# Performance work log

Measured on AMD Instinct MI355X. Metric: run time of the kernel, lower is better.

## Reference

```python
import jax, jax.numpy as jnp
import numpy as np

B, D, E, K, H, C = 8192, 1024, 8, 2, 2048, 512
LN_EPS = 1e-5


def setup_inputs() -> dict:
    key = jax.random.key(0)
    ks = jax.random.split(key, 6)
    s = 0.02
    return {
        "x": jax.random.normal(ks[0], (B, D), dtype=jnp.float32),
        "Wr": jax.random.normal(ks[1], (E, D), dtype=jnp.float32) * s,  # router weight [E,D]
        "br": jnp.zeros((E,), dtype=jnp.float32),
        "gamma": jnp.ones((E, D), dtype=jnp.float32),   # per-expert LayerNorm scale
        "beta": jnp.zeros((E, D), dtype=jnp.float32),   # per-expert LayerNorm shift
        "W1": jax.random.normal(ks[2], (E, H, D), dtype=jnp.float32) * s,
        "b1": jnp.zeros((E, H), dtype=jnp.float32),
        "W2": jax.random.normal(ks[3], (E, C, H), dtype=jnp.float32) * s,
        "b2": jnp.zeros((E, C), dtype=jnp.float32),
    }


def reference(x, Wr, br, gamma, beta, W1, b1, W2, b2):
    # Router + top-k gating (softmax over the k selected logits only)
    router_logits = x @ Wr.T + br                       # [B,E]
    topk_vals, topk_idx = jax.lax.top_k(router_logits, K)  # [B,K]
    topk_w = jax.nn.softmax(topk_vals, axis=-1)         # [B,K]
    # Dense gate [B,E]: gate[b,e] = sum_j topk_w[b,j] * (topk_idx[b,j]==e)
    gate = (jax.nn.one_hot(topk_idx, E, dtype=x.dtype) * topk_w[..., None]).sum(axis=1)

    # LayerNorm statistics are expert-independent; affine is per-expert
    mu = x.mean(axis=-1, keepdims=True)
    var = ((x - mu) ** 2).mean(axis=-1, keepdims=True)
    xn = (x - mu) * jax.lax.rsqrt(var + LN_EPS)          # [B,D]

    out = jnp.zeros((x.shape[0], C), dtype=x.dtype)
    for e in range(E):  # small fixed expert count
        xe = xn * gamma[e] + beta[e]                     # [B,D]
        h = jax.nn.gelu(xe @ W1[e].T + b1[e], approximate=False)  # [B,H]
        y = h @ W2[e].T + b2[e]                          # [B,C]
        out = out + gate[:, e:e + 1] * y
    return out
```

## Files before the change

### kernel.cpp

```cpp
#include <hip/hip_runtime.h>
#include <hip/hip_bf16.h>
#include <math.h>

#define B_TOK 8192
#define DDIM 1024
#define NEXP 8
#define HDIM 2048
#define CDIM 512
#define LN_EPS 1e-5f
#define MAXT256 72
#define MAXROWS (MAXT256 * 256)

typedef __attribute__((ext_vector_type(4))) float f32x4;
typedef __attribute__((ext_vector_type(8))) short bf16x8;

__device__ __forceinline__ unsigned short f2bf(float f) {
  __hip_bfloat16 h = __float2bfloat16(f);
  return *reinterpret_cast<unsigned short*>(&h);
}
__device__ __forceinline__ float bf2f(unsigned short u) {
  unsigned int x = ((unsigned int)u) << 16;
  return *reinterpret_cast<float*>(&x);
}

__device__ __forceinline__ float gelu_f(float v) {
  const float t = __builtin_fmaf(0.044715f * v, v, 1.0f);
  const float u = -1.5957691216f * v * t;
  return v * __builtin_amdgcn_rcpf(1.0f + __expf(u));
}

__device__ __forceinline__ void gload_lds16(const unsigned short* g, unsigned short* l) {
  __builtin_amdgcn_global_load_lds(
      (const __attribute__((address_space(1))) unsigned int*)g,
      (__attribute__((address_space(3))) unsigned int*)l, 16, 0, 0);
}

__global__ __launch_bounds__(256) void router_ln_kernel(
    const float* __restrict__ x, const float* __restrict__ Wr,
    const float* __restrict__ br, int* __restrict__ eidx,
    float* __restrict__ wgt, unsigned short* __restrict__ xn) {
  const int wid = threadIdx.x >> 6;
  const int lane = threadIdx.x & 63;
  const int tok = blockIdx.x * 4 + wid;

  const float4* xr = reinterpret_cast<const float4*>(x + (size_t)tok * DDIM);
  float4 xv[4];
  float sum = 0.f, sumsq = 0.f;
  float dot[NEXP];
#pragma unroll
  for (int e = 0; e < NEXP; ++e) dot[e] = 0.f;

#pragma unroll
  for (int i = 0; i < 4; ++i) {
    const int f = i * 64 + lane;
    float4 v = xr[f];
    xv[i] = v;
    sum += v.x + v.y + v.z + v.w;
    sumsq += v.x * v.x + v.y * v.y + v.z * v.z + v.w * v.w;
#pragma unroll
    for (int e = 0; e < NEXP; ++e) {
      float4 w = reinterpret_cast<const float4*>(Wr + e * DDIM)[f];
      dot[e] += v.x * w.x + v.y * w.y + v.z * w.z + v.w * w.w;
    }
  }
#pragma unroll
  for (int off = 32; off > 0; off >>= 1) {
    sum += __shfl_xor(sum, off);
    sumsq += __shfl_xor(sumsq, off);
#pragma unroll
    for (int e = 0; e < NEXP; ++e) dot[e] += __shfl_xor(dot[e], off);
  }
  const float mu = sum * (1.f / DDIM);
  const float var = sumsq * (1.f / DDIM) - mu * mu;
  const float rs = rsqrtf(var + LN_EPS);

  float lg[NEXP];
#pragma unroll
  for (int e = 0; e < NEXP; ++e) lg[e] = dot[e] + br[e];

  int i1 = 0; float v1 = lg[0];
#pragma unroll
  for (int e = 1; e < NEXP; ++e) { if (lg[e] > v1) { v1 = lg[e]; i1 = e; } }
  int i2 = -1; float v2 = -3.4e38f;
#pragma unroll
  for (int e = 0; e < NEXP; ++e) { if (e != i1 && lg[e] > v2) { v2 = lg[e]; i2 = e; } }

  const float e2 = __expf(v2 - v1);
  const float inv = 1.f / (1.f + e2);
  if (lane == 0) {
    eidx[tok * 2] = i1; eidx[tok * 2 + 1] = i2;
    wgt[tok * 2] = inv; wgt[tok * 2 + 1] = e2 * inv;
  }

  unsigned short* xnr = xn + (size_t)tok * DDIM;
#pragma unroll
  for (int i = 0; i < 4; ++i) {
    const int f = i * 64 + lane;
    float4 v = xv[i];
    ushort4 o;
    o.x = f2bf((v.x - mu) * rs);
    o.y = f2bf((v.y - mu) * rs);
    o.z = f2bf((v.z - mu) * rs);
    o.w = f2bf((v.w - mu) * rs);
    reinterpret_cast<ushort4*>(xnr)[f] = o;
  }
}

__global__ __launch_bounds__(256) void sort_kernel(
    const int* __restrict__ eidx,
    int* __restrict__ tokRow,
    int* __restrict__ slot2row,
    int* __restrict__ tileExp,
    int* __restrict__ nTilesOut) {
  __shared__ int cnt[NEXP], segBase[NEXP], cur[NEXP];
  const int tid = threadIdx.x;
  if (tid < NEXP) { cnt[tid] = 0; cur[tid] = 0; }
  __syncthreads();
  for (int t = tid; t < B_TOK * 2; t += 256)
    atomicAdd(&cnt[eidx[t]], 1);
  __syncthreads();
  if (tid == 0) {
    int c = 0;
    for (int e = 0; e < NEXP; ++e) {
      segBase[e] = c;
      const int nt = (cnt[e] + 255) >> 8;
      for (int t = 0; t < nt; ++t) tileExp[(c >> 8) + t] = e;
      for (int p = c + cnt[e]; p < c + nt * 256; ++p) tokRow[p] = 0;
      c += nt * 256;
    }
    *nTilesOut = c >> 8;
  }
  __syncthreads();
  for (int t = tid; t < B_TOK * 2; t += 256) {
    const int e = eidx[t];
    const int pos = segBase[e] + atomicAdd(&cur[e], 1);
    tokRow[pos] = t >> 1;
    slot2row[t] = pos;
  }
}

__global__ __launch_bounds__(256) void prep_w1_kernel(
    const float* __restrict__ W1, const float* __restrict__ gamma,
    const float* __restrict__ beta, const float* __restrict__ b1,
    unsigned short* __restrict__ W1g, float* __restrict__ c1) {
  const int eh = blockIdx.x;
  const int e = eh >> 11;
  const int tid = threadIdx.x;

  float4 w = reinterpret_cast<const float4*>(W1 + (size_t)eh * DDIM)[tid];
  float4 g = reinterpret_cast<const float4*>(gamma + (size_t)e * DDIM)[tid];
  float4 bt = reinterpret_cast<const float4*>(beta + (size_t)e * DDIM)[tid];

  ushort4 o;
  o.x = f2bf(w.x * g.x); o.y = f2bf(w.y * g.y);
  o.z = f2bf(w.z * g.z); o.w = f2bf(w.w * g.w);
  reinterpret_cast<ushort4*>(W1g + (size_t)eh * DDIM)[tid] = o;

  float p = w.x * bt.x + w.y * bt.y + w.z * bt.z + w.w * bt.w;
#pragma unroll
  for (int off = 32; off > 0; off >>= 1) p += __shfl_xor(p, off);
  __shared__ float red[4];
  const int lane = tid & 63, wv = tid >> 6;
  if (lane == 0) red[wv] = p;
  __syncthreads();
  if (tid == 0) c1[eh] = b1[eh] + red[0] + red[1] + red[2] + red[3];
}

__global__ __launch_bounds__(256) void prep_w2_kernel(
    const float* __restrict__ W2, unsigned short* __restrict__ W2b) {
  const int idx = blockIdx.x * 256 + threadIdx.x;
  float4 w = reinterpret_cast<const float4*>(W2)[idx];
  ushort4 o;
  o.x = f2bf(w.x); o.y = f2bf(w.y); o.z = f2bf(w.z); o.w = f2bf(w.w);
  reinterpret_cast<ushort4*>(W2b)[idx] = o;
}

#define BM 128
#define BN 128
#define BKK 64

__global__ __launch_bounds__(256) void gemm1_gelu_kernel(
    const unsigned short* __restrict__ A,
    const unsigned short* __restrict__ W1g,
    const float* __restrict__ c1,
    const int* __restrict__ tokRow, const int* __restrict__ tileExp,
    const int* __restrict__ nTiles,
    unsigned short* __restrict__ Hout) {
  const int flat = blockIdx.x;
  const int by = flat & 15;
  const int bx = flat >> 4;
  if ((bx >> 1) >= *nTiles) return;
  const int e = tileExp[bx >> 1];

  __shared__ unsigned short lA[BM * BKK];
  __shared__ unsigned short lB[BN * BKK];
  const int tid = threadIdx.x;
  const int lane = tid & 63;
  const int wid = tid >> 6;
  const int wr = wid >> 1, wc = wid & 1;
  const int l15 = lane & 15, l4 = lane >> 4;

  const unsigned short* Bbase = W1g + ((size_t)e * HDIM + (size_t)by * BN) * DDIM;

  const int r = tid >> 3;
  const int swz = ((tid & 7) ^ (r & 7)) * 8;
  const int dst = (tid & 7) * 8;

  const unsigned short* aP[4];
  const unsigned short* bP[4];
#pragma unroll
  for (int i = 0; i < 4; ++i) {
    aP[i] = A + (size_t)tokRow[bx * BM + i * 32 + r] * DDIM + swz;
    bP[i] = Bbase + (size_t)(i * 32 + r) * DDIM + swz;
  }

  f32x4 acc[4][4];
#pragma unroll
  for (int n = 0; n < 4; ++n)
#pragma unroll
    for (int m = 0; m < 4; ++m)
#pragma unroll
      for (int j = 0; j < 4; ++j) acc[n][m][j] = 0.f;

#pragma unroll 1
  for (int it = 0; it < DDIM / BKK; ++it) {
#pragma unroll
    for (int i = 0; i < 4; ++i)
      gload_lds16(aP[i], &lA[(i * 32 + r) * BKK + dst]);
#pragma unroll
    for (int i = 0; i < 4; ++i)
      gload_lds16(bP[i], &lB[(i * 32 + r) * BKK + dst]);
    __syncthreads();
#pragma unroll
    for (int kk = 0; kk < 2; ++kk) {
      bf16x8 xf[4], wf[4];
      const int slot = (((kk * 4 + l4) ^ (l15 & 7)) * 8);
#pragma unroll
      for (int m = 0; m < 4; ++m)
        xf[m] = *reinterpret_cast<const bf16x8*>(
            &lA[(wr * 64 + m * 16 + l15) * BKK + slot]);
#pragma unroll
      for (int n = 0; n < 4; ++n)
        wf[n] = *reinterpret_cast<const bf16x8*>(
            &lB[(wc * 64 + n * 16 + l15) * BKK + slot]);
#pragma unroll
      for (int n = 0; n < 4; ++n)
#pragma unroll
        for (int m = 0; m < 4; ++m)
          acc[n][m] = __builtin_amdgcn_mfma_f32_16x16x32_bf16(wf[n], xf[m], acc[n][m], 0, 0, 0);
    }
    __syncthreads();
#pragma unroll
    for (int i = 0; i < 4; ++i) { aP[i] += BKK; bP[i] += BKK; }
  }

  const int row0 = bx * BM + wr * 64;
  const int col0 = by * BN + wc * 64;
  const float* biasp = c1 + e * HDIM;
#pragma unroll
  for (int n = 0; n < 4; ++n) {
    const int hb = col0 + n * 16 + l4 * 4;
    const float4 b4 = *reinterpret_cast<const float4*>(biasp + hb);
#pragma unroll
    for (int m = 0; m < 4; ++m) {
      const int tokr = row0 + m * 16 + l15;
      ushort4 o;
      o.x = f2bf(gelu_f(acc[n][m][0] + b4.x));
      o.y = f2bf(gelu_f(acc[n][m][1] + b4.y));
      o.z = f2bf(gelu_f(acc[n][m][2] + b4.z));
      o.w = f2bf(gelu_f(acc[n][m][3] + b4.w));
      *reinterpret_cast<ushort4*>(&Hout[(size_t)tokr * HDIM + hb]) = o;
    }
  }
}

__global__ __launch_bounds__(256) void gemm2_kernel(
    const unsigned short* __restrict__ Hbuf,
    const unsigned short* __restrict__ W2b,
    const int* __restrict__ tileExp, const int* __restrict__ nTiles,
    unsigned short* __restrict__ Y) {
  const int flat = blockIdx.x;
  const int p = flat & 7;
  const int q = flat >> 3;
  const int by = p >> 1;
  const int bx = (p & 1) * 72 + q;
  if ((bx >> 1) >= *nTiles) return;
  const int e = tileExp[bx >> 1];

  __shared__ unsigned short lA[BM * BKK];
  __shared__ unsigned short lB[BN * BKK];
  const int tid = threadIdx.x;
  const int lane = tid & 63;
  const int wid = tid >> 6;
  const int wr = wid >> 1, wc = wid & 1;
  const int l15 = lane & 15, l4 = lane >> 4;

  const unsigned short* Abase = Hbuf + (size_t)bx * BM * HDIM;
  const unsigned short* Bbase = W2b + ((size_t)e * CDIM + (size_t)by * BN) * HDIM;

  f32x4 acc[4][4];
#pragma unroll
  for (int n = 0; n < 4; ++n)
#pragma unroll
    for (int m = 0; m < 4; ++m)
#pragma unroll
      for (int j = 0; j < 4; ++j) acc[n][m][j] = 0.f;

  const int r = tid >> 3;
  const int swz = ((tid & 7) ^ (r & 7)) * 8;
  const int dst = (tid & 7) * 8;

  for (int k0 = 0; k0 < HDIM; k0 += BKK) {
#pragma unroll
    for (int i = 0; i < 4; ++i)
      gload_lds16(Abase + (size_t)(i * 32 + r) * HDIM + k0 + swz,
                  &lA[(i * 32 + r) * BKK + dst]);
#pragma unroll
    for (int i = 0; i < 4; ++i)
      gload_lds16(Bbase + (size_t)(i * 32 + r) * HDIM + k0 + swz,
                  &lB[(i * 32 + r) * BKK + dst]);
    __syncthreads();
#pragma unroll
    for (int kk = 0; kk < 2; ++kk) {
      bf16x8 xf[4], wf[4];
      const int slot = (((kk * 4 + l4) ^ (l15 & 7)) * 8);
#pragma unroll
      for (int m = 0; m < 4; ++m)
        xf[m] = *reinterpret_cast<const bf16x8*>(
            &lA[(wr * 64 + m * 16 + l15) * BKK + slot]);
#pragma unroll
      for (int n = 0; n < 4; ++n)
        wf[n] = *reinterpret_cast<const bf16x8*>(
            &lB[(wc * 64 + n * 16 + l15) * BKK + slot]);
#pragma unroll
      for (int n = 0; n < 4; ++n)
#pragma unroll
        for (int m = 0; m < 4; ++m)
          acc[n][m] = __builtin_amdgcn_mfma_f32_16x16x32_bf16(wf[n], xf[m], acc[n][m], 0, 0, 0);
    }
    __syncthreads();
  }

  const int row0 = bx * BM + wr * 64;
  const int col0 = by * BN + wc * 64;
#pragma unroll
  for (int n = 0; n < 4; ++n) {
    const int cb = col0 + n * 16 + l4 * 4;
#pragma unroll
    for (int m = 0; m < 4; ++m) {
      const int tokr = row0 + m * 16 + l15;
      ushort4 o;
      o.x = f2bf(acc[n][m][0]);
      o.y = f2bf(acc[n][m][1]);
      o.z = f2bf(acc[n][m][2]);
      o.w = f2bf(acc[n][m][3]);
      *reinterpret_cast<ushort4*>(&Y[(size_t)tokr * CDIM + cb]) = o;
    }
  }
}

__global__ __launch_bounds__(256) void combine_kernel(
    const unsigned short* __restrict__ Y, const int* __restrict__ slot2row,
    const int* __restrict__ eidx, const float* __restrict__ wgt,
    const float* __restrict__ b2, float* __restrict__ out) {
  const int idx = blockIdx.x * 256 + threadIdx.x;
  const int b = idx >> 7;
  const int c4 = (idx & 127) * 4;
  const int r0 = slot2row[b * 2], r1 = slot2row[b * 2 + 1];
  const int e0 = eidx[b * 2], e1 = eidx[b * 2 + 1];
  const float w0 = wgt[b * 2], w1 = wgt[b * 2 + 1];
  ushort4 y0 = *reinterpret_cast<const ushort4*>(Y + (size_t)r0 * CDIM + c4);
  ushort4 y1 = *reinterpret_cast<const ushort4*>(Y + (size_t)r1 * CDIM + c4);
  float4 bb0 = *reinterpret_cast<const float4*>(b2 + e0 * CDIM + c4);
  float4 bb1 = *reinterpret_cast<const float4*>(b2 + e1 * CDIM + c4);
  float4 o;
  o.x = w0 * (bf2f(y0.x) + bb0.x) + w1 * (bf2f(y1.x) + bb1.x);
  o.y = w0 * (bf2f(y0.y) + bb0.y) + w1 * (bf2f(y1.y) + bb1.y);
  o.z = w0 * (bf2f(y0.z) + bb0.z) + w1 * (bf2f(y1.z) + bb1.z);
  o.w = w0 * (bf2f(y0.w) + bb0.w) + w1 * (bf2f(y1.w) + bb1.w);
  *reinterpret_cast<float4*>(out + (size_t)b * CDIM + c4) = o;
}

extern "C" void kernel_launch(void* const* d_in, const int* in_sizes, int n_in,
                              void* d_out, int out_size, void* d_ws, size_t ws_size,
                              hipStream_t stream) {
  const float* x     = (const float*)d_in[0];
  const float* Wr    = (const float*)d_in[1];
  const float* br    = (const float*)d_in[2];
  const float* gamma = (const float*)d_in[3];
  const float* beta  = (const float*)d_in[4];
  const float* W1    = (const float*)d_in[5];
  const float* b1    = (const float*)d_in[6];
  const float* W2    = (const float*)d_in[7];
  const float* b2    = (const float*)d_in[8];
  float* out = (float*)d_out;

  char* ws = (char*)d_ws;
  unsigned short* xn   = (unsigned short*)(ws);
  unsigned short* W2b  = (unsigned short*)(ws);
  unsigned short* hbuf = (unsigned short*)(ws + (size_t)16 * 1048576);
  unsigned short* W1g  = (unsigned short*)(ws + (size_t)88 * 1048576);
  unsigned short* ybuf = (unsigned short*)(ws + (size_t)88 * 1048576);
  char* misc           = ws + (size_t)120 * 1048576;
  float* c1      = (float*)(misc);
  int* eidx      = (int*)(misc + 65536);
  float* wgt     = (float*)(misc + 2 * 65536);
  int* slot2row  = (int*)(misc + 3 * 65536);
  int* tokRow    = (int*)(misc + 4 * 65536);
  int* tileExp   = (int*)(misc + 4 * 65536 + 131072);
  int* nTiles    = tileExp + MAXT256;

  router_ln_kernel<<<dim3(B_TOK / 4), dim3(256), 0, stream>>>(x, Wr, br, eidx, wgt, xn);
  sort_kernel<<<dim3(1), dim3(256), 0, stream>>>(eidx, tokRow, slot2row, tileExp, nTiles);
  prep_w1_kernel<<<dim3(NEXP * HDIM), dim3(256), 0, stream>>>(W1, gamma, beta, b1, W1g, c1);

  gemm1_gelu_kernel<<<dim3(2304), dim3(256), 0, stream>>>(
      xn, W1g, c1, tokRow, tileExp, nTiles, hbuf);

  prep_w2_kernel<<<dim3((NEXP * CDIM * HDIM / 4) / 256), dim3(256), 0, stream>>>(W2, W2b);

  gemm2_kernel<<<dim3(576), dim3(256), 0, stream>>>(
      hbuf, W2b, tileExp, nTiles, ybuf);
  combine_kernel<<<dim3(B_TOK * CDIM / 4 / 256), dim3(256), 0, stream>>>(
      ybuf, slot2row, eidx, wgt, b2, out);
}
```

Before: 268.6 us.

## Double-buffer LDS tiles in GEMM1 with async global-to-LDS prefetch

The GEMM1+GELU kernel now uses two LDS buffers for the A and B tiles and issues direct global-to-LDS loads two K-steps ahead. Explicit vmcnt waits and raw s_barrier replace __syncthreads, so the loads for the next tile overlap with the MFMA work on the current one. LDS usage doubles to 64 KB per block, which may reduce occupancy. Correctness depends on the hand-written waitcnt counts and barrier placement.

```diff
diff --git a/kernel.cpp b/kernel.cpp
--- a/kernel.cpp
+++ b/kernel.cpp
@@ -192,8 +192,8 @@
   if ((bx >> 1) >= *nTiles) return;
   const int e = tileExp[bx >> 1];
 
-  __shared__ unsigned short lA[BM * BKK];
-  __shared__ unsigned short lB[BN * BKK];
+  __shared__ unsigned short lA[2][BM * BKK];
+  __shared__ unsigned short lB[2][BN * BKK];
   const int tid = threadIdx.x;
   const int lane = tid & 63;
   const int wid = tid >> 6;
@@ -222,15 +222,26 @@
 #pragma unroll
       for (int j = 0; j < 4; ++j) acc[n][m][j] = 0.f;
 
+  auto stage = [&](int b, int k0) {
+#pragma unroll
+    for (int i = 0; i < 4; ++i)
+      gload_lds16(aP[i] + k0, &lA[b][(i * 32 + r) * BKK + dst]);
+#pragma unroll
+    for (int i = 0; i < 4; ++i)
+      gload_lds16(bP[i] + k0, &lB[b][(i * 32 + r) * BKK + dst]);
+  };
+
+  stage(0, 0);
+  stage(1, BKK);
+
 #pragma unroll 1
-  for (int it = 0; it < DDIM / BKK; ++it) {
-#pragma unroll
-    for (int i = 0; i < 4; ++i)
-      gload_lds16(aP[i], &lA[(i * 32 + r) * BKK + dst]);
-#pragma unroll
-    for (int i = 0; i < 4; ++i)
-      gload_lds16(bP[i], &lB[(i * 32 + r) * BKK + dst]);
-    __syncthreads();
+  for (int it = 0; it < 16; ++it) {
+    if (it < 15) asm volatile("s_waitcnt vmcnt(8)" ::: "memory");
+    else         asm volatile("s_waitcnt vmcnt(0)" ::: "memory");
+    __builtin_amdgcn_sched_barrier(0);
+    asm volatile("s_barrier" ::: "memory");
+    const unsigned short* la = lA[it & 1];
+    const unsigned short* lb = lB[it & 1];
 #pragma unroll
     for (int kk = 0; kk < 2; ++kk) {
       bf16x8 xf[4], wf[4];
@@ -238,20 +249,19 @@
 #pragma unroll
       for (int m = 0; m < 4; ++m)
         xf[m] = *reinterpret_cast<const bf16x8*>(
-            &lA[(wr * 64 + m * 16 + l15) * BKK + slot]);
+            &la[(wr * 64 + m * 16 + l15) * BKK + slot]);
 #pragma unroll
       for (int n = 0; n < 4; ++n)
         wf[n] = *reinterpret_cast<const bf16x8*>(
-            &lB[(wc * 64 + n * 16 + l15) * BKK + slot]);
+            &lb[(wc * 64 + n * 16 + l15) * BKK + slot]);
 #pragma unroll
       for (int n = 0; n < 4; ++n)
 #pragma unroll
         for (int m = 0; m < 4; ++m)
           acc[n][m] = __builtin_amdgcn_mfma_f32_16x16x32_bf16(wf[n], xf[m], acc[n][m], 0, 0, 0);
     }
-    __syncthreads();
-#pragma unroll
-    for (int i = 0; i < 4; ++i) { aP[i] += BKK; bP[i] += BKK; }
+    asm volatile("s_barrier" ::: "memory");
+    if (it < 14) stage(it & 1, (it + 2) * BKK);
   }
 
   const int row0 = bx * BM + wr * 64;
```

Result: no change. 263.7 us (median of 2 runs) (-1.8%).
